# Kernel tuning notes

Hardware: AMD Instinct MI355X
Metric: run time of the kernel (lower is better)

## Reference

```python
import jax, jax.numpy as jnp
import numpy as np

HEADS = 8
DIM_HEAD = 64
DIM = 512
MAX_POS_EMB = 512
SCALE = DIM_HEAD ** -0.5


def setup_inputs() -> dict:
    key = jax.random.key(0)
    ks = jax.random.split(key, 6)
    B, N = 2, 2048
    inner = HEADS * DIM_HEAD  # 512
    x = jax.random.normal(ks[0], (B, N, DIM), dtype=jnp.float32)
    # torch Linear weights stored as [out, in]; we keep [in, out] for x @ W
    Wq = jax.random.normal(ks[1], (DIM, inner), dtype=jnp.float32) * (DIM ** -0.5)
    Wkv = jax.random.normal(ks[2], (DIM, 2 * inner), dtype=jnp.float32) * (DIM ** -0.5)
    Wo = jax.random.normal(ks[3], (inner, DIM), dtype=jnp.float32) * (inner ** -0.5)
    bo = jax.random.normal(ks[4], (DIM,), dtype=jnp.float32) * 0.02
    rel_emb = jax.random.normal(ks[5], (2 * MAX_POS_EMB + 1, DIM_HEAD), dtype=jnp.float32)
    return {"x": x, "Wq": Wq, "Wkv": Wkv, "Wo": Wo, "bo": bo, "rel_emb": rel_emb}


def reference(x, Wq, Wkv, Wo, bo, rel_emb):
    B, N, _ = x.shape
    h, d = HEADS, DIM_HEAD
    q = x @ Wq                                # [B, N, h*d]
    kv = x @ Wkv                              # [B, N, 2*h*d]
    k, v = jnp.split(kv, 2, axis=-1)
    to_heads = lambda t: t.reshape(B, N, h, d).transpose(0, 2, 1, 3)  # [B, h, N, d]
    q, k, v = to_heads(q), to_heads(k), to_heads(v)

    dots = jnp.einsum('bhid,bhjd->bhij', q, k) * SCALE  # [B, h, N, N]

    # relative positional bias: dist clamped to [-max, max], shifted to [0, 2*max]
    seq = jnp.arange(N)
    dist = jnp.clip(seq[:, None] - seq[None, :], -MAX_POS_EMB, MAX_POS_EMB) + MAX_POS_EMB
    rel = rel_emb[dist]                                 # [N, N, d]
    pos_attn = jnp.einsum('bhnd,njd->bhnj', q, rel) * SCALE
    dots = dots + pos_attn

    attn = jax.nn.softmax(dots, axis=-1)
    out = jnp.einsum('bhij,bhjd->bhid', attn, v)        # [B, h, N, d]
    out = out.transpose(0, 2, 1, 3).reshape(B, N, h * d)
    return out @ Wo + bo
```

## Files before the change

kernel.cpp:

```cpp
#include <hip/hip_runtime.h>
#include <hip/hip_bf16.h>
#include <stdint.h>

#define HEADS 8
#define DHEAD 64
#define DIM 512
#define NSEQ 2048
#define BATCH 2
#define NROWS (BATCH * NSEQ)
#define QKV_N 1536
#define REL_ROWS 1025
#define REL_PITCH 1088
#define NSPLIT 2
#define KV_PER_SPLIT (NSEQ / NSPLIT)

static constexpr float SCALE_LOG2E = 0.125f * 1.4426950408889634f;

typedef __attribute__((ext_vector_type(8))) short bf16x8;
typedef __attribute__((ext_vector_type(4))) float f32x4;

__device__ __forceinline__ uint16_t f2bf(float f) {
    union { float f; uint32_t u; } v{f};
    uint32_t r = (v.u + 0x7FFFu + ((v.u >> 16) & 1u)) >> 16;
    return (uint16_t)r;
}
__device__ __forceinline__ float bf2f(uint16_t u) {
    union { uint32_t u; float f; } v{(uint32_t)u << 16};
    return v.f;
}

__global__ void prep_misc(const float* __restrict__ x, const float* __restrict__ rel,
                          uint16_t* __restrict__ xb, uint16_t* __restrict__ relb) {
    int total = NROWS * DIM + REL_PITCH * DHEAD;
    for (int idx = blockIdx.x * blockDim.x + threadIdx.x; idx < total; idx += gridDim.x * blockDim.x) {
        if (idx < NROWS * DIM) {
            xb[idx] = f2bf(x[idx]);
        } else {
            int i2 = idx - NROWS * DIM;
            relb[i2] = (i2 < REL_ROWS * DHEAD) ? f2bf(rel[i2]) : (uint16_t)0;
        }
    }
}

__global__ void prep_w(const float* __restrict__ Wq, const float* __restrict__ Wkv,
                       const float* __restrict__ Wo,
                       uint16_t* __restrict__ Wqkv_t, uint16_t* __restrict__ Wo_t) {
    __shared__ float tile[32][33];
    int bid = blockIdx.x;
    const float* src; uint16_t* dst; int J, ti, tj;
    if (bid < 256)      { src = Wq;  dst = Wqkv_t;             J = 512;  ti = bid >> 4;        tj = bid & 15; }
    else if (bid < 768) { int b = bid - 256; src = Wkv; dst = Wqkv_t + 512 * 512; J = 1024; ti = b >> 5; tj = b & 31; }
    else                { int b = bid - 768; src = Wo;  dst = Wo_t;   J = 512;  ti = b >> 4;        tj = b & 15; }
    int tx = threadIdx.x & 31, ty = threadIdx.x >> 5;
    int k0 = ti * 32, j0 = tj * 32;
    #pragma unroll
    for (int i = 0; i < 4; i++) tile[ty + 8 * i][tx] = src[(size_t)(k0 + ty + 8 * i) * J + j0 + tx];
    __syncthreads();
    #pragma unroll
    for (int i = 0; i < 4; i++) dst[(size_t)(j0 + ty + 8 * i) * 512 + k0 + tx] = f2bf(tile[tx][ty + 8 * i]);
}

template <bool BF16_OUT>
__global__ __launch_bounds__(256) void gemm128(const uint16_t* __restrict__ A,
                                               const uint16_t* __restrict__ Bt,
                                               void* __restrict__ Cout,
                                               const float* __restrict__ bias,
                                               int K, int ldc) {
    __shared__ char lds[32768];
    char* ldsA = lds;
    char* ldsB = lds + 16384;
    int m0 = blockIdx.x * 128, n0 = blockIdx.y * 128;
    int t = threadIdx.x, lane = t & 63, w = t >> 6;
    int wr = w >> 1, wc = w & 1;
    int l15 = lane & 15, lh = lane >> 4;
    f32x4 acc[4][4] = {};
    for (int k0 = 0; k0 < K; k0 += 64) {
        __syncthreads();
        {
            int row = t >> 3, ch = t & 7;
            #pragma unroll
            for (int p = 0; p < 4; p++) {
                int r = row + 32 * p;
                bf16x8 va = *(const bf16x8*)(A + (size_t)(m0 + r) * K + k0 + ch * 8);
                *(bf16x8*)(ldsA + r * 128 + ((ch * 16) ^ ((r & 7) << 4))) = va;
                bf16x8 vb = *(const bf16x8*)(Bt + (size_t)(n0 + r) * K + k0 + ch * 8);
                *(bf16x8*)(ldsB + r * 128 + ((ch * 16) ^ ((r & 7) << 4))) = vb;
            }
        }
        __syncthreads();
        #pragma unroll
        for (int kk = 0; kk < 2; kk++) {
            bf16x8 a[4], b[4];
            #pragma unroll
            for (int mi = 0; mi < 4; mi++) {
                int m = wr * 64 + mi * 16 + l15;
                a[mi] = *(const bf16x8*)(ldsA + m * 128 + ((kk * 64 + lh * 16) ^ ((m & 7) << 4)));
            }
            #pragma unroll
            for (int ni = 0; ni < 4; ni++) {
                int n = wc * 64 + ni * 16 + l15;
                b[ni] = *(const bf16x8*)(ldsB + n * 128 + ((kk * 64 + lh * 16) ^ ((n & 7) << 4)));
            }
            #pragma unroll
            for (int mi = 0; mi < 4; mi++)
                #pragma unroll
                for (int ni = 0; ni < 4; ni++)
                    acc[mi][ni] = __builtin_amdgcn_mfma_f32_16x16x32_bf16(a[mi], b[ni], acc[mi][ni], 0, 0, 0);
        }
    }
    #pragma unroll
    for (int mi = 0; mi < 4; mi++)
        #pragma unroll
        for (int ni = 0; ni < 4; ni++)
            #pragma unroll
            for (int i = 0; i < 4; i++) {
                int m = m0 + wr * 64 + mi * 16 + lh * 4 + i;
                int n = n0 + wc * 64 + ni * 16 + l15;
                float v = acc[mi][ni][i];
                if constexpr (BF16_OUT) ((uint16_t*)Cout)[(size_t)m * ldc + n] = f2bf(v);
                else                    ((float*)Cout)[(size_t)m * ldc + n] = v + bias[n];
            }
}

__global__ __launch_bounds__(256) void qrel_gemm(const uint16_t* __restrict__ QKV,
                                                 const uint16_t* __restrict__ relb,
                                                 uint16_t* __restrict__ qrel) {
    __shared__ char lds[16384];
    char* ldsA = lds;
    char* ldsB = lds + 8192;
    int h = blockIdx.y;
    int r0 = blockIdx.x * 64;
    int t = threadIdx.x, lane = t & 63, w = t >> 6;
    int l15 = lane & 15, lh = lane >> 4;
    {
        int row = t >> 3, ch = t & 7;
        #pragma unroll
        for (int p = 0; p < 2; p++) {
            int r = row + 32 * p;
            bf16x8 v = *(const bf16x8*)(QKV + (size_t)(r0 + r) * QKV_N + h * 64 + ch * 8);
            *(bf16x8*)(ldsA + r * 128 + ((ch * 16) ^ ((r & 7) << 4))) = v;
        }
    }
    __syncthreads();
    bf16x8 afrag[2];
    #pragma unroll
    for (int kk = 0; kk < 2; kk++) {
        int m = w * 16 + l15;
        afrag[kk] = *(const bf16x8*)(ldsA + m * 128 + ((kk * 64 + lh * 16) ^ ((m & 7) << 4)));
    }
    for (int pb = 0; pb < REL_PITCH / 64; pb++) {
        int p0 = pb * 64;
        __syncthreads();
        {
            int row = t >> 3, ch = t & 7;
            #pragma unroll
            for (int p = 0; p < 2; p++) {
                int r = row + 32 * p;
                bf16x8 v = *(const bf16x8*)(relb + (size_t)(p0 + r) * 64 + ch * 8);
                *(bf16x8*)(ldsB + r * 128 + ((ch * 16) ^ ((r & 7) << 4))) = v;
            }
        }
        __syncthreads();
        f32x4 acc[4] = {};
        #pragma unroll
        for (int kk = 0; kk < 2; kk++)
            #pragma unroll
            for (int ni = 0; ni < 4; ni++) {
                int n = ni * 16 + l15;
                bf16x8 b = *(const bf16x8*)(ldsB + n * 128 + ((kk * 64 + lh * 16) ^ ((n & 7) << 4)));
                acc[ni] = __builtin_amdgcn_mfma_f32_16x16x32_bf16(afrag[kk], b, acc[ni], 0, 0, 0);
            }
        #pragma unroll
        for (int ni = 0; ni < 4; ni++)
            #pragma unroll
            for (int i = 0; i < 4; i++) {
                int rr = r0 + w * 16 + lh * 4 + i;
                int p = p0 + ni * 16 + l15;
                qrel[((size_t)h * NROWS + rr) * REL_PITCH + p] = f2bf(acc[ni][i]);
            }
    }
}

__global__ __launch_bounds__(512, 4) void attn_kernel(const uint16_t* __restrict__ QKV,
                                                      const uint16_t* __restrict__ qrel,
                                                      float* __restrict__ Opart,
                                                      float* __restrict__ mlpart) {
    __shared__ char lds[65536];
    char* ldsQ = lds;
    char* ldsKV = lds + 16384;
    char* ldsP = lds + 49152;
    int qb = blockIdx.x, h = blockIdx.y;
    int b = blockIdx.z >> 1, sp = blockIdx.z & 1;
    int t = threadIdx.x, lane = t & 63, w = t >> 6;
    int l15 = lane & 15, lh = lane >> 4;
    int row = t >> 3, ch = t & 7;
    int n0 = qb * 128;
    int kvbase = sp * KV_PER_SPLIT;
    size_t rowQ = (size_t)b * NSEQ + n0;

    {
        #pragma unroll
        for (int p = 0; p < 2; p++) {
            int r = row + 64 * p;
            bf16x8 v = *(const bf16x8*)(QKV + (rowQ + r) * QKV_N + h * 64 + ch * 8);
            *(bf16x8*)(ldsQ + r * 128 + ((ch * 16) ^ ((r & 7) << 4))) = v;
        }
    }
    __syncthreads();
    bf16x8 qf[2];
    #pragma unroll
    for (int kk = 0; kk < 2; kk++) {
        int m = w * 16 + l15;
        qf[kk] = *(const bf16x8*)(ldsQ + m * 128 + ((kk * 64 + lh * 16) ^ ((m & 7) << 4)));
    }

    f32x4 oacc[4] = {};
    float mrow[4], lrow[4];
    #pragma unroll
    for (int i = 0; i < 4; i++) { mrow[i] = -INFINITY; lrow[i] = 0.f; }
    const uint16_t* qrel_base = qrel + ((size_t)h * NROWS + (size_t)b * NSEQ) * REL_PITCH;
    char* myP = ldsP + w * 2048;

    bf16x8 kreg, vreg;
    {
        size_t gro = ((size_t)b * NSEQ + kvbase + row) * QKV_N + h * 64 + ch * 8;
        kreg = *(const bf16x8*)(QKV + gro + 512);
        vreg = *(const bf16x8*)(QKV + gro + 1024);
    }

    const int NT = KV_PER_SPLIT / 64;
    for (int tt = 0; tt < NT; ++tt) {
        char* ldsK = ldsKV + (tt & 1) * 16384;
        char* ldsV = ldsK + 8192;
        *(bf16x8*)(ldsK + row * 128 + ((ch * 16) ^ ((row & 7) << 4))) = kreg;
        #pragma unroll
        for (int dd = 0; dd < 8; dd++) {
            int d = ch * 8 + dd;
            int s = dd ^ ch;
            *(uint16_t*)(ldsV + d * 128 + 2 * (row ^ (s << 3))) = (uint16_t)vreg[dd];
        }
        __syncthreads();
        if (tt + 1 < NT) {
            size_t gro = ((size_t)b * NSEQ + kvbase + (tt + 1) * 64 + row) * QKV_N + h * 64 + ch * 8;
            kreg = *(const bf16x8*)(QKV + gro + 512);
            vreg = *(const bf16x8*)(QKV + gro + 1024);
        }
        int kv0 = kvbase + tt * 64;

        uint16_t g[16];
        #pragma unroll
        for (int nf = 0; nf < 4; nf++) {
            int j = kv0 + nf * 16 + l15;
            #pragma unroll
            for (int i = 0; i < 4; i++) {
                int n = n0 + w * 16 + lh * 4 + i;
                int d = n - j;
                d = d < -512 ? -512 : (d > 512 ? 512 : d);
                g[nf * 4 + i] = qrel_base[(size_t)n * REL_PITCH + d + 512];
            }
        }

        f32x4 sacc[4] = {};
        #pragma unroll
        for (int kk = 0; kk < 2; kk++)
            #pragma unroll
            for (int nf = 0; nf < 4; nf++) {
                int n = nf * 16 + l15;
                bf16x8 bfv = *(const bf16x8*)(ldsK + n * 128 + ((kk * 64 + lh * 16) ^ ((n & 7) << 4)));
                sacc[nf] = __builtin_amdgcn_mfma_f32_16x16x32_bf16(qf[kk], bfv, sacc[nf], 0, 0, 0);
            }

        #pragma unroll
        for (int nf = 0; nf < 4; nf++)
            #pragma unroll
            for (int i = 0; i < 4; i++)
                sacc[nf][i] += bf2f(g[nf * 4 + i]);

        float alpha[4];
        #pragma unroll
        for (int i = 0; i < 4; i++) {
            float mx = fmaxf(fmaxf(sacc[0][i], sacc[1][i]), fmaxf(sacc[2][i], sacc[3][i]));
            #pragma unroll
            for (int off = 1; off < 16; off <<= 1) mx = fmaxf(mx, __shfl_xor(mx, off));
            float mnew = fmaxf(mrow[i], mx);
            alpha[i] = exp2f((mrow[i] - mnew) * SCALE_LOG2E);
            mrow[i] = mnew;
            float rs = 0.f;
            int r = lh * 4 + i;
            #pragma unroll
            for (int nf = 0; nf < 4; nf++) {
                float p = exp2f((sacc[nf][i] - mnew) * SCALE_LOG2E);
                rs += p;
                int col = nf * 16 + l15;
                *(uint16_t*)(myP + r * 128 + ((col * 2) ^ ((r & 7) << 4))) = f2bf(p);
            }
            #pragma unroll
            for (int off = 1; off < 16; off <<= 1) rs += __shfl_xor(rs, off);
            lrow[i] = lrow[i] * alpha[i] + rs;
        }
        #pragma unroll
        for (int nf = 0; nf < 4; nf++)
            #pragma unroll
            for (int i = 0; i < 4; i++)
                oacc[nf][i] *= alpha[i];

        asm volatile("s_waitcnt lgkmcnt(0)" ::: "memory");
        #pragma unroll
        for (int kk = 0; kk < 2; kk++) {
            bf16x8 pa = *(const bf16x8*)(myP + l15 * 128 + ((kk * 64 + lh * 16) ^ ((l15 & 7) << 4)));
            #pragma unroll
            for (int nf = 0; nf < 4; nf++) {
                int d = nf * 16 + l15;
                int sd = (d & 7) ^ ((d >> 3) & 7);
                bf16x8 vb = *(const bf16x8*)(ldsV + d * 128 + 16 * ((kk * 4 + lh) ^ sd));
                oacc[nf] = __builtin_amdgcn_mfma_f32_16x16x32_bf16(pa, vb, oacc[nf], 0, 0, 0);
            }
        }
    }

    size_t rbase = ((size_t)(sp * BATCH + b) * HEADS + h) * NSEQ;
    #pragma unroll
    for (int nf = 0; nf < 4; nf++)
        #pragma unroll
        for (int i = 0; i < 4; i++) {
            int r = n0 + w * 16 + lh * 4 + i;
            Opart[(rbase + r) * 64 + nf * 16 + l15] = oacc[nf][i];
        }
    if (l15 == 0) {
        #pragma unroll
        for (int i = 0; i < 4; i++) {
            int r = n0 + w * 16 + lh * 4 + i;
            mlpart[(rbase + r) * 2]     = mrow[i];
            mlpart[(rbase + r) * 2 + 1] = lrow[i];
        }
    }
}

__global__ __launch_bounds__(256) void combine_kernel(const float* __restrict__ Opart,
                                                      const float* __restrict__ mlpart,
                                                      uint16_t* __restrict__ attO) {
    int lane = threadIdx.x & 63;
    int R = blockIdx.x * 4 + (threadIdx.x >> 6);
    const int SPSTRIDE = BATCH * HEADS * NSEQ;
    float m1 = mlpart[(size_t)R * 2], l1 = mlpart[(size_t)R * 2 + 1];
    float m2 = mlpart[((size_t)SPSTRIDE + R) * 2], l2 = mlpart[((size_t)SPSTRIDE + R) * 2 + 1];
    float M = fmaxf(m1, m2);
    float w1 = exp2f((m1 - M) * SCALE_LOG2E);
    float w2 = exp2f((m2 - M) * SCALE_LOG2E);
    float Linv = 1.f / (l1 * w1 + l2 * w2);
    float o1 = Opart[(size_t)R * 64 + lane];
    float o2 = Opart[((size_t)SPSTRIDE + R) * 64 + lane];
    float o = (o1 * w1 + o2 * w2) * Linv;
    int bh = R >> 11, n = R & 2047;
    int b = bh >> 3, hh = bh & 7;
    attO[((size_t)(b * NSEQ + n)) * DIM + hh * 64 + lane] = f2bf(o);
}

extern "C" void kernel_launch(void* const* d_in, const int* in_sizes, int n_in,
                              void* d_out, int out_size, void* d_ws, size_t ws_size,
                              hipStream_t stream) {
    const float* x   = (const float*)d_in[0];
    const float* Wq  = (const float*)d_in[1];
    const float* Wkv = (const float*)d_in[2];
    const float* Wo  = (const float*)d_in[3];
    const float* bo  = (const float*)d_in[4];
    const float* rel = (const float*)d_in[5];
    char* ws = (char*)d_ws;
    uint16_t* Xb     = (uint16_t*)(ws);
    float*    mlp    = (float*)(ws);
    uint16_t* Wqkv_t = (uint16_t*)(ws + 4194304);
    uint16_t* Wo_t   = (uint16_t*)(ws + 5767168);
    uint16_t* relb   = (uint16_t*)(ws + 6291456);
    uint16_t* QKV    = (uint16_t*)(ws + 6430720);
    uint16_t* attO   = (uint16_t*)(ws + 19013632);
    uint16_t* qrel   = (uint16_t*)(ws + 23207936);
    float*    Opart  = (float*)(ws + 94511104);

    prep_misc<<<2048, 256, 0, stream>>>(x, rel, Xb, relb);
    prep_w<<<1024, 256, 0, stream>>>(Wq, Wkv, Wo, Wqkv_t, Wo_t);
    gemm128<true><<<dim3(32, 12), 256, 0, stream>>>(Xb, Wqkv_t, QKV, nullptr, 512, QKV_N);
    qrel_gemm<<<dim3(64, 8), 256, 0, stream>>>(QKV, relb, qrel);
    attn_kernel<<<dim3(16, 8, 4), 512, 0, stream>>>(QKV, qrel, Opart, mlp);
    combine_kernel<<<8192, 256, 0, stream>>>(Opart, mlp, attO);
    gemm128<false><<<dim3(32, 4), 256, 0, stream>>>(attO, Wo_t, (float*)d_out, bo, 512, DIM);
}
```

Measured before the change: 162.0 us.

## Restructure attention kernel: smaller blocks, transposed S, lazy rescale, prefetched bias

Rewrites the attention kernel to use 256-thread blocks over 64 query rows, with a swizzled block index so that neighbouring blocks share K/V in cache. S is computed transposed so that each lane owns one query row, which makes the softmax reductions cheaper. Rescaling of the running max is skipped unless the new max exceeds the old one by a threshold, and P is packed to bf16 with a hardware convert instruction. The relative-bias gather and the K/V loads are prefetched one tile ahead, with constant fast paths for fully clamped tiles, and MFMA sections get a higher wave priority. In exchange the kernel carries more registers and more complex control flow.

```diff
diff --git a/kernel.cpp b/kernel.cpp
--- a/kernel.cpp
+++ b/kernel.cpp
@@ -27,6 +27,11 @@
 __device__ __forceinline__ float bf2f(uint16_t u) {
     union { uint32_t u; float f; } v{(uint32_t)u << 16};
     return v.f;
+}
+__device__ __forceinline__ uint32_t cvt_pk_bf16(float lo, float hi) {
+    uint32_t r;
+    asm("v_cvt_pk_bf16_f32 %0, %1, %2" : "=v"(r) : "v"(lo), "v"(hi));
+    return r;
 }
 
 __global__ void prep_misc(const float* __restrict__ x, const float* __restrict__ rel,
@@ -181,30 +186,30 @@
     }
 }
 
-__global__ __launch_bounds__(512, 4) void attn_kernel(const uint16_t* __restrict__ QKV,
+__global__ __launch_bounds__(256, 4) void attn_kernel(const uint16_t* __restrict__ QKV,
                                                       const uint16_t* __restrict__ qrel,
                                                       float* __restrict__ Opart,
                                                       float* __restrict__ mlpart) {
-    __shared__ char lds[65536];
+    __shared__ char lds[40960];
     char* ldsQ = lds;
-    char* ldsKV = lds + 16384;
-    char* ldsP = lds + 49152;
-    int qb = blockIdx.x, h = blockIdx.y;
-    int b = blockIdx.z >> 1, sp = blockIdx.z & 1;
+    char* ldsKV = lds + 8192;
+
+    int flat = blockIdx.x + 32 * (blockIdx.y + 8 * blockIdx.z);
+    int x = (flat & 7) * 128 + (flat >> 3);
+    int qb = x & 31, h = (x >> 5) & 7, z = x >> 8;
+    int b = z >> 1, sp = z & 1;
+
     int t = threadIdx.x, lane = t & 63, w = t >> 6;
     int l15 = lane & 15, lh = lane >> 4;
-    int row = t >> 3, ch = t & 7;
-    int n0 = qb * 128;
+    int sr = t >> 2, sc = t & 3;
+    int n0 = qb * 64;
     int kvbase = sp * KV_PER_SPLIT;
     size_t rowQ = (size_t)b * NSEQ + n0;
 
-    {
-        #pragma unroll
-        for (int p = 0; p < 2; p++) {
-            int r = row + 64 * p;
-            bf16x8 v = *(const bf16x8*)(QKV + (rowQ + r) * QKV_N + h * 64 + ch * 8);
-            *(bf16x8*)(ldsQ + r * 128 + ((ch * 16) ^ ((r & 7) << 4))) = v;
-        }
+    #pragma unroll
+    for (int p = 0; p < 2; p++) {
+        bf16x8 v = *(const bf16x8*)(QKV + (rowQ + sr) * QKV_N + h * 64 + sc * 16 + 8 * p);
+        *(bf16x8*)(ldsQ + sr * 128 + ((sc * 32 + 16 * p) ^ ((sr & 7) << 4))) = v;
     }
     __syncthreads();
     bf16x8 qf[2];
@@ -213,98 +218,135 @@
         int m = w * 16 + l15;
         qf[kk] = *(const bf16x8*)(ldsQ + m * 128 + ((kk * 64 + lh * 16) ^ ((m & 7) << 4)));
     }
+    char* myP = ldsQ + w * 2048;
 
     f32x4 oacc[4] = {};
-    float mrow[4], lrow[4];
-    #pragma unroll
-    for (int i = 0; i < 4; i++) { mrow[i] = -INFINITY; lrow[i] = 0.f; }
-    const uint16_t* qrel_base = qrel + ((size_t)h * NROWS + (size_t)b * NSEQ) * REL_PITCH;
-    char* myP = ldsP + w * 2048;
-
-    bf16x8 kreg, vreg;
+    float mrow = -INFINITY, lrow = 0.f;
+    int nrow = n0 + w * 16 + l15;
+    const uint16_t* qrow = qrel + ((size_t)h * NROWS + (size_t)b * NSEQ + nrow) * REL_PITCH + 512;
+
+    auto load_kv = [&](int tile, bf16x8* kr, bf16x8* vr) {
+        size_t gro = ((size_t)b * NSEQ + kvbase + tile * 64 + sr) * QKV_N + h * 64 + sc * 16;
+        kr[0] = *(const bf16x8*)(QKV + gro + 512);
+        kr[1] = *(const bf16x8*)(QKV + gro + 520);
+        vr[0] = *(const bf16x8*)(QKV + gro + 1024);
+        vr[1] = *(const bf16x8*)(QKV + gro + 1032);
+    };
+    auto scatter_kv = [&](int tile, bf16x8* kr, bf16x8* vr) {
+        char* ldsK = ldsKV + (tile & 1) * 16384;
+        char* ldsV = ldsK + 8192;
+        #pragma unroll
+        for (int p = 0; p < 2; p++)
+            *(bf16x8*)(ldsK + sr * 128 + ((sc * 32 + 16 * p) ^ ((sr & 7) << 4))) = kr[p];
+        #pragma unroll
+        for (int p = 0; p < 2; p++)
+            #pragma unroll
+            for (int dd = 0; dd < 8; dd++) {
+                int d = sc * 16 + 8 * p + dd;
+                int sd = dd ^ ((sc * 2 + p) & 7);
+                *(uint16_t*)(ldsV + d * 128 + 2 * (sr ^ (sd << 3))) = (uint16_t)vr[p][dd];
+            }
+    };
+    auto load_g = [&](int tile, uint16_t* g) {
+        int kv0 = kvbase + tile * 64;
+        int rel0 = n0 - kv0;
+        if (rel0 <= -575) {
+            uint16_t v = qrow[-512];
+            #pragma unroll
+            for (int e = 0; e < 16; e++) g[e] = v;
+        } else if (rel0 >= 575) {
+            uint16_t v = qrow[512];
+            #pragma unroll
+            for (int e = 0; e < 16; e++) g[e] = v;
+        } else {
+            int nmk = nrow - kv0;
+            #pragma unroll
+            for (int nf = 0; nf < 4; nf++)
+                #pragma unroll
+                for (int i = 0; i < 4; i++) {
+                    int dj = nmk - (nf * 16 + lh * 4 + i);
+                    dj = dj < -512 ? -512 : (dj > 512 ? 512 : dj);
+                    g[nf * 4 + i] = qrow[dj];
+                }
+        }
+    };
+
+    const int NT = KV_PER_SPLIT / 64;
+    uint16_t gA[16], gB[16];
     {
-        size_t gro = ((size_t)b * NSEQ + kvbase + row) * QKV_N + h * 64 + ch * 8;
-        kreg = *(const bf16x8*)(QKV + gro + 512);
-        vreg = *(const bf16x8*)(QKV + gro + 1024);
-    }
-
-    const int NT = KV_PER_SPLIT / 64;
-    for (int tt = 0; tt < NT; ++tt) {
+        bf16x8 kr[2], vr[2];
+        load_kv(0, kr, vr);
+        load_g(0, gA);
+        scatter_kv(0, kr, vr);
+    }
+
+    auto body = [&](int tt, uint16_t* gCur, uint16_t* gNext) {
         char* ldsK = ldsKV + (tt & 1) * 16384;
         char* ldsV = ldsK + 8192;
-        *(bf16x8*)(ldsK + row * 128 + ((ch * 16) ^ ((row & 7) << 4))) = kreg;
-        #pragma unroll
-        for (int dd = 0; dd < 8; dd++) {
-            int d = ch * 8 + dd;
-            int s = dd ^ ch;
-            *(uint16_t*)(ldsV + d * 128 + 2 * (row ^ (s << 3))) = (uint16_t)vreg[dd];
-        }
         __syncthreads();
-        if (tt + 1 < NT) {
-            size_t gro = ((size_t)b * NSEQ + kvbase + (tt + 1) * 64 + row) * QKV_N + h * 64 + ch * 8;
-            kreg = *(const bf16x8*)(QKV + gro + 512);
-            vreg = *(const bf16x8*)(QKV + gro + 1024);
-        }
-        int kv0 = kvbase + tt * 64;
-
-        uint16_t g[16];
-        #pragma unroll
-        for (int nf = 0; nf < 4; nf++) {
-            int j = kv0 + nf * 16 + l15;
-            #pragma unroll
-            for (int i = 0; i < 4; i++) {
-                int n = n0 + w * 16 + lh * 4 + i;
-                int d = n - j;
-                d = d < -512 ? -512 : (d > 512 ? 512 : d);
-                g[nf * 4 + i] = qrel_base[(size_t)n * REL_PITCH + d + 512];
-            }
-        }
+        bf16x8 kr[2], vr[2];
+        bool pf = (tt + 1 < NT);
+        if (pf) { load_kv(tt + 1, kr, vr); load_g(tt + 1, gNext); }
 
         f32x4 sacc[4] = {};
+        __builtin_amdgcn_s_setprio(1);
         #pragma unroll
         for (int kk = 0; kk < 2; kk++)
             #pragma unroll
             for (int nf = 0; nf < 4; nf++) {
                 int n = nf * 16 + l15;
-                bf16x8 bfv = *(const bf16x8*)(ldsK + n * 128 + ((kk * 64 + lh * 16) ^ ((n & 7) << 4)));
-                sacc[nf] = __builtin_amdgcn_mfma_f32_16x16x32_bf16(qf[kk], bfv, sacc[nf], 0, 0, 0);
-            }
+                bf16x8 kf = *(const bf16x8*)(ldsK + n * 128 + ((kk * 64 + lh * 16) ^ ((n & 7) << 4)));
+                sacc[nf] = __builtin_amdgcn_mfma_f32_16x16x32_bf16(kf, qf[kk], sacc[nf], 0, 0, 0);
+            }
+        __builtin_amdgcn_s_setprio(0);
 
         #pragma unroll
         for (int nf = 0; nf < 4; nf++)
             #pragma unroll
             for (int i = 0; i < 4; i++)
-                sacc[nf][i] += bf2f(g[nf * 4 + i]);
-
-        float alpha[4];
-        #pragma unroll
-        for (int i = 0; i < 4; i++) {
-            float mx = fmaxf(fmaxf(sacc[0][i], sacc[1][i]), fmaxf(sacc[2][i], sacc[3][i]));
-            #pragma unroll
-            for (int off = 1; off < 16; off <<= 1) mx = fmaxf(mx, __shfl_xor(mx, off));
-            float mnew = fmaxf(mrow[i], mx);
-            alpha[i] = exp2f((mrow[i] - mnew) * SCALE_LOG2E);
-            mrow[i] = mnew;
-            float rs = 0.f;
-            int r = lh * 4 + i;
-            #pragma unroll
-            for (int nf = 0; nf < 4; nf++) {
-                float p = exp2f((sacc[nf][i] - mnew) * SCALE_LOG2E);
-                rs += p;
-                int col = nf * 16 + l15;
-                *(uint16_t*)(myP + r * 128 + ((col * 2) ^ ((r & 7) << 4))) = f2bf(p);
-            }
-            #pragma unroll
-            for (int off = 1; off < 16; off <<= 1) rs += __shfl_xor(rs, off);
-            lrow[i] = lrow[i] * alpha[i] + rs;
-        }
+                sacc[nf][i] += bf2f(gCur[nf * 4 + i]);
+
+        float mx = sacc[0][0];
         #pragma unroll
         for (int nf = 0; nf < 4; nf++)
             #pragma unroll
-            for (int i = 0; i < 4; i++)
-                oacc[nf][i] *= alpha[i];
+            for (int i = 0; i < 4; i++) mx = fmaxf(mx, sacc[nf][i]);
+        mx = fmaxf(mx, __shfl_xor(mx, 16));
+        mx = fmaxf(mx, __shfl_xor(mx, 32));
+        bool resc = !__all(mx <= mrow + 64.0f);
+        float alpha = 1.0f;
+        if (resc) {
+            float mnew = fmaxf(mrow, mx);
+            alpha = exp2f((mrow - mnew) * SCALE_LOG2E);
+            mrow = mnew;
+        }
+        float rs = 0.f;
+        int pbase = l15 * 128, sw = (l15 & 7) << 4;
+        #pragma unroll
+        for (int nf = 0; nf < 4; nf++) {
+            float p0 = exp2f((sacc[nf][0] - mrow) * SCALE_LOG2E);
+            float p1 = exp2f((sacc[nf][1] - mrow) * SCALE_LOG2E);
+            float p2 = exp2f((sacc[nf][2] - mrow) * SCALE_LOG2E);
+            float p3 = exp2f((sacc[nf][3] - mrow) * SCALE_LOG2E);
+            rs += (p0 + p1) + (p2 + p3);
+            int c2 = (nf * 16 + lh * 4) * 2;
+            *(uint32_t*)(myP + pbase + (c2 ^ sw))       = cvt_pk_bf16(p0, p1);
+            *(uint32_t*)(myP + pbase + ((c2 + 4) ^ sw)) = cvt_pk_bf16(p2, p3);
+        }
+        rs += __shfl_xor(rs, 16);
+        rs += __shfl_xor(rs, 32);
+        lrow = lrow * alpha + rs;
+        if (resc) {
+            #pragma unroll
+            for (int i = 0; i < 4; i++) {
+                float ai = __shfl(alpha, lh * 4 + i);
+                #pragma unroll
+                for (int nf = 0; nf < 4; nf++) oacc[nf][i] *= ai;
+            }
+        }
 
         asm volatile("s_waitcnt lgkmcnt(0)" ::: "memory");
+        __builtin_amdgcn_s_setprio(1);
         #pragma unroll
         for (int kk = 0; kk < 2; kk++) {
             bf16x8 pa = *(const bf16x8*)(myP + l15 * 128 + ((kk * 64 + lh * 16) ^ ((l15 & 7) << 4)));
@@ -316,6 +358,14 @@
                 oacc[nf] = __builtin_amdgcn_mfma_f32_16x16x32_bf16(pa, vb, oacc[nf], 0, 0, 0);
             }
         }
+        __builtin_amdgcn_s_setprio(0);
+        if (pf) scatter_kv(tt + 1, kr, vr);
+    };
+
+    #pragma unroll 1
+    for (int tt2 = 0; tt2 < NT; tt2 += 2) {
+        body(tt2, gA, gB);
+        body(tt2 + 1, gB, gA);
     }
 
     size_t rbase = ((size_t)(sp * BATCH + b) * HEADS + h) * NSEQ;
@@ -326,13 +376,9 @@
             int r = n0 + w * 16 + lh * 4 + i;
             Opart[(rbase + r) * 64 + nf * 16 + l15] = oacc[nf][i];
         }
-    if (l15 == 0) {
-        #pragma unroll
-        for (int i = 0; i < 4; i++) {
-            int r = n0 + w * 16 + lh * 4 + i;
-            mlpart[(rbase + r) * 2]     = mrow[i];
-            mlpart[(rbase + r) * 2 + 1] = lrow[i];
-        }
+    if (lh == 0) {
+        mlpart[(rbase + nrow) * 2]     = mrow;
+        mlpart[(rbase + nrow) * 2 + 1] = lrow;
     }
 }
 
@@ -380,7 +426,7 @@
     prep_w<<<1024, 256, 0, stream>>>(Wq, Wkv, Wo, Wqkv_t, Wo_t);
     gemm128<true><<<dim3(32, 12), 256, 0, stream>>>(Xb, Wqkv_t, QKV, nullptr, 512, QKV_N);
     qrel_gemm<<<dim3(64, 8), 256, 0, stream>>>(QKV, relb, qrel);
-    attn_kernel<<<dim3(16, 8, 4), 512, 0, stream>>>(QKV, qrel, Opart, mlp);
+    attn_kernel<<<dim3(32, 8, 4), 256, 0, stream>>>(QKV, qrel, Opart, mlp);
     combine_kernel<<<8192, 256, 0, stream>>>(Opart, mlp, attO);
     gemm128<false><<<dim3(32, 4), 256, 0, stream>>>(attO, Wo_t, (float*)d_out, bo, 512, DIM);
 }
```

After: 176.9 us. 9.2% more time.

## Software-pipeline attention loop with lazy rescale and MFMA-computed row sums

Applied to the files above, without the earlier changes.

Restructures the attention inner loop so the next tile's K/V and relative-bias gathers are issued before the current tile's compute, and the LDS scatter happens after the PV MFMAs. Row sums are obtained by appending a ones column to V (a fifth MFMA output block), which removes the shuffle reductions. The max rescale is skipped when the new scores stay within a threshold of the running max. Bias gathers are collapsed to a single value per row for tiles fully in the clamped region. The P buffer now reuses the Q region, which shrinks LDS, and s_setprio is placed around the MFMA sections. The trade-off is an extra MFMA per kk step, higher register pressure, and reliance on the lazy-rescale threshold staying numerically safe.

```diff
diff --git a/kernel.cpp b/kernel.cpp
--- a/kernel.cpp
+++ b/kernel.cpp
@@ -185,10 +185,9 @@
                                                       const uint16_t* __restrict__ qrel,
                                                       float* __restrict__ Opart,
                                                       float* __restrict__ mlpart) {
-    __shared__ char lds[65536];
+    __shared__ char lds[53248];
     char* ldsQ = lds;
     char* ldsKV = lds + 16384;
-    char* ldsP = lds + 49152;
     int qb = blockIdx.x, h = blockIdx.y;
     int b = blockIdx.z >> 1, sp = blockIdx.z & 1;
     int t = threadIdx.x, lane = t & 63, w = t >> 6;
@@ -199,12 +198,18 @@
     size_t rowQ = (size_t)b * NSEQ + n0;
 
     {
-        #pragma unroll
-        for (int p = 0; p < 2; p++) {
-            int r = row + 64 * p;
-            bf16x8 v = *(const bf16x8*)(QKV + (rowQ + r) * QKV_N + h * 64 + ch * 8);
-            *(bf16x8*)(ldsQ + r * 128 + ((ch * 16) ^ ((r & 7) << 4))) = v;
-        }
+        int buf = t >> 8, idx = t & 255;
+        uint32_t val = (idx < 16) ? 0x3F803F80u : 0u;
+        char* p = ldsKV + buf * 18432 + 8192 + 8192 + (idx >> 4) * 128 + (idx & 15) * 8;
+        *(uint32_t*)(p) = val;
+        *(uint32_t*)(p + 4) = val;
+    }
+
+    #pragma unroll
+    for (int p = 0; p < 2; p++) {
+        int r = row + 64 * p;
+        bf16x8 v = *(const bf16x8*)(QKV + (rowQ + r) * QKV_N + h * 64 + ch * 8);
+        *(bf16x8*)(ldsQ + r * 128 + ((ch * 16) ^ ((r & 7) << 4))) = v;
     }
     __syncthreads();
     bf16x8 qf[2];
@@ -213,109 +218,153 @@
         int m = w * 16 + l15;
         qf[kk] = *(const bf16x8*)(ldsQ + m * 128 + ((kk * 64 + lh * 16) ^ ((m & 7) << 4)));
     }
-
-    f32x4 oacc[4] = {};
-    float mrow[4], lrow[4];
-    #pragma unroll
-    for (int i = 0; i < 4; i++) { mrow[i] = -INFINITY; lrow[i] = 0.f; }
-    const uint16_t* qrel_base = qrel + ((size_t)h * NROWS + (size_t)b * NSEQ) * REL_PITCH;
-    char* myP = ldsP + w * 2048;
-
-    bf16x8 kreg, vreg;
-    {
-        size_t gro = ((size_t)b * NSEQ + kvbase + row) * QKV_N + h * 64 + ch * 8;
-        kreg = *(const bf16x8*)(QKV + gro + 512);
-        vreg = *(const bf16x8*)(QKV + gro + 1024);
-    }
-
-    const int NT = KV_PER_SPLIT / 64;
-    for (int tt = 0; tt < NT; ++tt) {
-        char* ldsK = ldsKV + (tt & 1) * 16384;
+    char* myP = ldsQ + w * 2048;
+
+    f32x4 oacc[5] = {};
+    float mrow[4];
+    #pragma unroll
+    for (int i = 0; i < 4; i++) mrow[i] = -INFINITY;
+
+    const uint16_t* qbase = qrel + ((size_t)h * NROWS + (size_t)b * NSEQ) * REL_PITCH;
+    uint32_t rowbase[4];
+    #pragma unroll
+    for (int i = 0; i < 4; i++) rowbase[i] = (uint32_t)(n0 + w * 16 + lh * 4 + i) * REL_PITCH + 512;
+
+    auto load_kv = [&](int tile, bf16x8& kr, bf16x8& vr) {
+        size_t gro = ((size_t)b * NSEQ + kvbase + tile * 64 + row) * QKV_N + h * 64 + ch * 8;
+        kr = *(const bf16x8*)(QKV + gro + 512);
+        vr = *(const bf16x8*)(QKV + gro + 1024);
+    };
+    auto scatter_kv = [&](int tile, bf16x8& kr, bf16x8& vr) {
+        char* ldsK = ldsKV + (tile & 1) * 18432;
         char* ldsV = ldsK + 8192;
-        *(bf16x8*)(ldsK + row * 128 + ((ch * 16) ^ ((row & 7) << 4))) = kreg;
+        *(bf16x8*)(ldsK + row * 128 + ((ch * 16) ^ ((row & 7) << 4))) = kr;
         #pragma unroll
         for (int dd = 0; dd < 8; dd++) {
             int d = ch * 8 + dd;
             int s = dd ^ ch;
-            *(uint16_t*)(ldsV + d * 128 + 2 * (row ^ (s << 3))) = (uint16_t)vreg[dd];
-        }
+            *(uint16_t*)(ldsV + d * 128 + 2 * (row ^ (s << 3))) = (uint16_t)vr[dd];
+        }
+    };
+    auto load_g = [&](int tile, uint16_t* g) {
+        int kv0 = kvbase + tile * 64;
+        int rel0 = n0 - kv0;
+        if (rel0 <= -640) {
+            #pragma unroll
+            for (int i = 0; i < 4; i++) {
+                uint16_t v = qbase[rowbase[i] - 512];
+                #pragma unroll
+                for (int nf = 0; nf < 4; nf++) g[nf * 4 + i] = v;
+            }
+        } else if (rel0 >= 576) {
+            #pragma unroll
+            for (int i = 0; i < 4; i++) {
+                uint16_t v = qbase[rowbase[i] + 512];
+                #pragma unroll
+                for (int nf = 0; nf < 4; nf++) g[nf * 4 + i] = v;
+            }
+        } else {
+            #pragma unroll
+            for (int i = 0; i < 4; i++) {
+                int nmk = (n0 + w * 16 + lh * 4 + i) - kv0;
+                #pragma unroll
+                for (int nf = 0; nf < 4; nf++) {
+                    int d = nmk - (nf * 16 + l15);
+                    d = d < -512 ? -512 : (d > 512 ? 512 : d);
+                    g[nf * 4 + i] = qbase[rowbase[i] + d];
+                }
+            }
+        }
+    };
+
+    const int NT = KV_PER_SPLIT / 64;
+    uint16_t gA[16], gB[16];
+    bf16x8 kreg, vreg;
+    load_kv(0, kreg, vreg);
+    load_g(0, gA);
+    scatter_kv(0, kreg, vreg);
+
+    auto body = [&](int tt, uint16_t* gCur, uint16_t* gNext) {
+        char* ldsK = ldsKV + (tt & 1) * 18432;
+        char* ldsV = ldsK + 8192;
         __syncthreads();
-        if (tt + 1 < NT) {
-            size_t gro = ((size_t)b * NSEQ + kvbase + (tt + 1) * 64 + row) * QKV_N + h * 64 + ch * 8;
-            kreg = *(const bf16x8*)(QKV + gro + 512);
-            vreg = *(const bf16x8*)(QKV + gro + 1024);
-        }
-        int kv0 = kvbase + tt * 64;
-
-        uint16_t g[16];
-        #pragma unroll
-        for (int nf = 0; nf < 4; nf++) {
-            int j = kv0 + nf * 16 + l15;
-            #pragma unroll
-            for (int i = 0; i < 4; i++) {
-                int n = n0 + w * 16 + lh * 4 + i;
-                int d = n - j;
-                d = d < -512 ? -512 : (d > 512 ? 512 : d);
-                g[nf * 4 + i] = qrel_base[(size_t)n * REL_PITCH + d + 512];
-            }
-        }
+        bool pf = (tt + 1 < NT);
+        if (pf) { load_kv(tt + 1, kreg, vreg); load_g(tt + 1, gNext); }
 
         f32x4 sacc[4] = {};
+        __builtin_amdgcn_s_setprio(1);
         #pragma unroll
         for (int kk = 0; kk < 2; kk++)
             #pragma unroll
             for (int nf = 0; nf < 4; nf++) {
                 int n = nf * 16 + l15;
-                bf16x8 bfv = *(const bf16x8*)(ldsK + n * 128 + ((kk * 64 + lh * 16) ^ ((n & 7) << 4)));
-                sacc[nf] = __builtin_amdgcn_mfma_f32_16x16x32_bf16(qf[kk], bfv, sacc[nf], 0, 0, 0);
-            }
+                bf16x8 kfv = *(const bf16x8*)(ldsK + n * 128 + ((kk * 64 + lh * 16) ^ ((n & 7) << 4)));
+                sacc[nf] = __builtin_amdgcn_mfma_f32_16x16x32_bf16(qf[kk], kfv, sacc[nf], 0, 0, 0);
+            }
+        __builtin_amdgcn_s_setprio(0);
 
         #pragma unroll
         for (int nf = 0; nf < 4; nf++)
             #pragma unroll
             for (int i = 0; i < 4; i++)
-                sacc[nf][i] += bf2f(g[nf * 4 + i]);
-
-        float alpha[4];
+                sacc[nf][i] += bf2f(gCur[nf * 4 + i]);
+
+        float lmax = sacc[0][0];
+        #pragma unroll
+        for (int nf = 0; nf < 4; nf++)
+            #pragma unroll
+            for (int i = 0; i < 4; i++) lmax = fmaxf(lmax, sacc[nf][i]);
+        float mmin = fminf(fminf(mrow[0], mrow[1]), fminf(mrow[2], mrow[3]));
+        if (!__all(lmax <= mmin + 64.0f)) {
+            #pragma unroll
+            for (int i = 0; i < 4; i++) {
+                float mx = fmaxf(fmaxf(sacc[0][i], sacc[1][i]), fmaxf(sacc[2][i], sacc[3][i]));
+                mx = fmaxf(mx, __shfl_xor(mx, 1));
+                mx = fmaxf(mx, __shfl_xor(mx, 2));
+                mx = fmaxf(mx, __shfl_xor(mx, 4));
+                mx = fmaxf(mx, __shfl_xor(mx, 8));
+                float mnew = fmaxf(mrow[i], mx);
+                float alpha = exp2f((mrow[i] - mnew) * SCALE_LOG2E);
+                mrow[i] = mnew;
+                #pragma unroll
+                for (int nf = 0; nf < 5; nf++) oacc[nf][i] *= alpha;
+            }
+        }
+
         #pragma unroll
         for (int i = 0; i < 4; i++) {
-            float mx = fmaxf(fmaxf(sacc[0][i], sacc[1][i]), fmaxf(sacc[2][i], sacc[3][i]));
-            #pragma unroll
-            for (int off = 1; off < 16; off <<= 1) mx = fmaxf(mx, __shfl_xor(mx, off));
-            float mnew = fmaxf(mrow[i], mx);
-            alpha[i] = exp2f((mrow[i] - mnew) * SCALE_LOG2E);
-            mrow[i] = mnew;
-            float rs = 0.f;
             int r = lh * 4 + i;
+            int rsw = (r & 7) << 4;
             #pragma unroll
             for (int nf = 0; nf < 4; nf++) {
-                float p = exp2f((sacc[nf][i] - mnew) * SCALE_LOG2E);
-                rs += p;
-                int col = nf * 16 + l15;
-                *(uint16_t*)(myP + r * 128 + ((col * 2) ^ ((r & 7) << 4))) = f2bf(p);
-            }
-            #pragma unroll
-            for (int off = 1; off < 16; off <<= 1) rs += __shfl_xor(rs, off);
-            lrow[i] = lrow[i] * alpha[i] + rs;
-        }
-        #pragma unroll
-        for (int nf = 0; nf < 4; nf++)
-            #pragma unroll
-            for (int i = 0; i < 4; i++)
-                oacc[nf][i] *= alpha[i];
+                float p = exp2f((sacc[nf][i] - mrow[i]) * SCALE_LOG2E);
+                uint32_t pb;
+                asm("v_cvt_pk_bf16_f32 %0, %1, %2" : "=v"(pb) : "v"(p), "v"(p));
+                *(uint16_t*)(myP + r * 128 + (((nf * 16 + l15) * 2) ^ rsw)) = (uint16_t)pb;
+            }
+        }
 
         asm volatile("s_waitcnt lgkmcnt(0)" ::: "memory");
+        __builtin_amdgcn_s_setprio(1);
         #pragma unroll
         for (int kk = 0; kk < 2; kk++) {
             bf16x8 pa = *(const bf16x8*)(myP + l15 * 128 + ((kk * 64 + lh * 16) ^ ((l15 & 7) << 4)));
             #pragma unroll
-            for (int nf = 0; nf < 4; nf++) {
+            for (int nf = 0; nf < 5; nf++) {
                 int d = nf * 16 + l15;
                 int sd = (d & 7) ^ ((d >> 3) & 7);
                 bf16x8 vb = *(const bf16x8*)(ldsV + d * 128 + 16 * ((kk * 4 + lh) ^ sd));
                 oacc[nf] = __builtin_amdgcn_mfma_f32_16x16x32_bf16(pa, vb, oacc[nf], 0, 0, 0);
             }
         }
+        __builtin_amdgcn_s_setprio(0);
+        if (pf) scatter_kv(tt + 1, kreg, vreg);
+    };
+
+    #pragma unroll 1
+    for (int tt2 = 0; tt2 < NT; tt2 += 2) {
+        body(tt2, gA, gB);
+        body(tt2 + 1, gB, gA);
     }
 
     size_t rbase = ((size_t)(sp * BATCH + b) * HEADS + h) * NSEQ;
@@ -331,7 +380,7 @@
         for (int i = 0; i < 4; i++) {
             int r = n0 + w * 16 + lh * 4 + i;
             mlpart[(rbase + r) * 2]     = mrow[i];
-            mlpart[(rbase + r) * 2 + 1] = lrow[i];
+            mlpart[(rbase + r) * 2 + 1] = oacc[4][i];
         }
     }
 }
```

After: 159.5 us. About the same (-1.6%).
